# Kernel tuning notes

Hardware: AMD Instinct MI355X
Metric: run time of the kernel (lower is better)

Reference implementation:

```python
import jax, jax.numpy as jnp
import numpy as np

B, S, H, P = 8, 2048, 256, 64
NQ = 20

def setup_inputs() -> dict:
    key = jax.random.key(0)
    ks = jax.random.split(key, 12)
    s = lambda fan_in: 1.0 / np.sqrt(fan_in)
    return {
        "feature_x": jax.random.normal(ks[0], (B, S, H), dtype=jnp.float32),
        "param_x": jax.random.normal(ks[1], (B, S, P), dtype=jnp.float32),
        "sim_w1": jax.random.uniform(ks[2], (H, H // 2), jnp.float32, -s(H), s(H)),
        "sim_b1": jax.random.uniform(ks[3], (H // 2,), jnp.float32, -s(H), s(H)),
        "sim_w2": jax.random.uniform(ks[4], (H // 2, 1), jnp.float32, -s(H // 2), s(H // 2)),
        "sim_b2": jax.random.uniform(ks[5], (1,), jnp.float32, -s(H // 2), s(H // 2)),
        "conf_w1": jax.random.uniform(ks[6], (H, H // 2), jnp.float32, -s(H), s(H)),
        "conf_b1": jax.random.uniform(ks[7], (H // 2,), jnp.float32, -s(H), s(H)),
        "conf_w2": jax.random.uniform(ks[8], (H // 2, 1), jnp.float32, -s(H // 2), s(H // 2)),
        "conf_b2": jax.random.uniform(ks[9], (1,), jnp.float32, -s(H // 2), s(H // 2)),
        "questions": jax.random.randint(ks[10], (B, S), 0, NQ, dtype=jnp.int64 if jax.config.jax_enable_x64 else jnp.int32),
    }

def _mlp_scalar(x, w1, b1, w2, b2):
    # [B,S,H] -> [B,S] (dropout is eval-mode identity)
    h = jax.nn.relu(jnp.einsum("bsh,hk->bsk", x, w1) + b1)
    return (jnp.einsum("bsk,ko->bso", h, w2) + b2)[..., 0]

def reference(feature_x, param_x, sim_w1, sim_b1, sim_w2, sim_b2,
              conf_w1, conf_b1, conf_w2, conf_b2, questions):
    similarities = _mlp_scalar(feature_x, sim_w1, sim_b1, sim_w2, sim_b2)          # [B,S]
    confidences = jax.nn.sigmoid(_mlp_scalar(feature_x, conf_w1, conf_b1, conf_w2, conf_b2))  # [B,S]
    # multiplicative equality mask (zeros, not -inf, outside group — faithful to source)
    qmask = (questions[:, :, None] == questions[:, None, :]).astype(feature_x.dtype)  # [B,S,S]
    logits = similarities[:, :, None] * qmask                                        # [B,i,j]
    attn = jax.nn.softmax(logits, axis=-2)                                           # softmax over i
    smoothed = jnp.einsum("bij,bip->bjp", attn, param_x)                              # attn^T @ param_x
    c = confidences[..., None]
    return c * param_x + (1.0 - c) * smoothed
```

## Files before the change

### kernel.cpp

```cpp
#include <hip/hip_runtime.h>
#include <math.h>

#define B_  8
#define S_  2048
#define H_  256
#define HK_ 128
#define P_  64
#define NQ_ 20
#define M_  (B_*S_)
#define ACC_STRIDE 2688

#define WS_SIM   0
#define WS_CONF  16384
#define WS_ACC   32768
#define WS_WT    54272

typedef __attribute__((ext_vector_type(8))) short bf16x8;
typedef __attribute__((ext_vector_type(4))) float f32x4;

__global__ void prep_kernel(const float* __restrict__ sw1, const float* __restrict__ cw1,
                            short* __restrict__ wtf, float* __restrict__ ws_acc)
{
    const int t = blockIdx.x * 256 + threadIdx.x;
    const int l = t & 63, nt = (t >> 6) & 7, kt = (t >> 9) & 7, mlp = t >> 12;
    const int col = l & 15, quad = l >> 4;
    const int n = nt * 16 + col;
    const float* w1 = mlp ? cw1 : sw1;
    short frag[8];
    #pragma unroll
    for (int j = 0; j < 8; ++j) {
        int k = kt * 32 + quad * 8 + j;
        union { float f; unsigned u; } c; c.f = w1[k * HK_ + n];
        frag[j] = (short)((c.u + 0x7FFF + ((c.u >> 16) & 1)) >> 16);
    }
    *(uint4*)(wtf + (size_t)t * 8) = *(const uint4*)frag;
    for (int s = t; s < B_ * ACC_STRIDE; s += 8192) ws_acc[s] = 0.f;
}

__launch_bounds__(256)
__global__ void mlp_mfma_kernel(const float* __restrict__ fx, const short* __restrict__ wtf,
                                const float* __restrict__ sb1, const float* __restrict__ sw2,
                                const float* __restrict__ sb2, const float* __restrict__ cb1,
                                const float* __restrict__ cw2, const float* __restrict__ cb2,
                                float* __restrict__ sim, float* __restrict__ conf)
{
    const int tid  = threadIdx.x;
    const int w    = tid >> 6, l = tid & 63;
    const int col  = l & 15, quad = l >> 4;
    const int mlp  = w >> 1, mt = w & 1;
    const int row  = blockIdx.x * 32 + mt * 16 + col;

    f32x4 acc[8];
    #pragma unroll
    for (int nt = 0; nt < 8; ++nt) acc[nt] = (f32x4){0.f, 0.f, 0.f, 0.f};

    const float* fxrow = fx + (size_t)row * H_;
    const short* wf = wtf + (size_t)mlp * 32768 + (size_t)l * 8;

    #pragma unroll
    for (int kt = 0; kt < 8; ++kt) {
        float4 a0 = *(const float4*)(fxrow + kt * 32 + quad * 8);
        float4 a1 = *(const float4*)(fxrow + kt * 32 + quad * 8 + 4);
        float af[8] = {a0.x, a0.y, a0.z, a0.w, a1.x, a1.y, a1.z, a1.w};
        bf16x8 ahi, alo;
        #pragma unroll
        for (int i = 0; i < 8; ++i) {
            union { float f; unsigned u; } c; c.f = af[i];
            unsigned hi = c.u >> 16;
            ahi[i] = (short)hi;
            union { float f; unsigned u; } h2; h2.u = hi << 16;
            union { float f; unsigned u; } c2; c2.f = af[i] - h2.f;
            alo[i] = (short)(c2.u >> 16);
        }
        const short* base = wf + (size_t)kt * 4096;
        #pragma unroll
        for (int nt = 0; nt < 8; ++nt) {
            bf16x8 bf = *(const bf16x8*)(base + nt * 512);
            acc[nt] = __builtin_amdgcn_mfma_f32_16x16x32_bf16(ahi, bf, acc[nt], 0, 0, 0);
            acc[nt] = __builtin_amdgcn_mfma_f32_16x16x32_bf16(alo, bf, acc[nt], 0, 0, 0);
        }
    }

    const float* b1 = mlp ? cb1 : sb1;
    const float* w2 = mlp ? cw2 : sw2;
    const float  b2v = mlp ? cb2[0] : sb2[0];
    float p[4] = {0.f, 0.f, 0.f, 0.f};
    #pragma unroll
    for (int nt = 0; nt < 8; ++nt) {
        float b1c = b1[nt * 16 + col];
        float w2c = w2[nt * 16 + col];
        #pragma unroll
        for (int j = 0; j < 4; ++j)
            p[j] += fmaxf(acc[nt][j] + b1c, 0.f) * w2c;
    }
    #pragma unroll
    for (int off = 8; off >= 1; off >>= 1)
        #pragma unroll
        for (int j = 0; j < 4; ++j) p[j] += __shfl_down(p[j], off, 16);

    if (col == 0) {
        #pragma unroll
        for (int j = 0; j < 4; ++j) {
            int r = blockIdx.x * 32 + mt * 16 + quad * 4 + j;
            float v = p[j] + b2v;
            if (mlp == 0) sim[r] = v;
            else          conf[r] = 1.0f / (1.0f + expf(-v));
        }
    }
}

__launch_bounds__(256)
__global__ void accum_kernel(const float* __restrict__ sim, const int* __restrict__ questions,
                             const float* __restrict__ px, float* __restrict__ ws_acc)
{
    const int b = blockIdx.x;
    const int chunk = blockIdx.y;
    const int tid = threadIdx.x;
    const int lane = tid & 63;
    const int g = tid >> 6;
    __shared__ float accs[4][ACC_STRIDE];
    for (int s = tid; s < 4 * ACC_STRIDE; s += 256) ((float*)accs)[s] = 0.f;
    __syncthreads();

    const float* simb = sim + b * S_;
    const int*   qb   = questions + b * S_;
    const float* pxb  = px + (size_t)b * S_ * P_;

    float Treg = 0.f;
    const int i0 = chunk * 64 + g;
    for (int t = 0; t < 16; ++t) {
        int i = i0 + 4 * t;
        int qi = qb[i];
        float e = expf(simb[i]);
        float v = pxb[(size_t)i * P_ + lane];
        Treg += v;
        accs[g][qi * 64 + lane]        += v;
        accs[g][(20 + qi) * 64 + lane] += e * v;
        if (lane == 0) {
            accs[g][2624 + qi] += e;
            accs[g][2644 + qi] += 1.0f;
        }
    }
    accs[g][2560 + lane] += Treg;
    __syncthreads();

    float* dst = ws_acc + (size_t)b * ACC_STRIDE;
    for (int s = tid; s < ACC_STRIDE; s += 256) {
        float sum = accs[0][s] + accs[1][s] + accs[2][s] + accs[3][s];
        atomicAdd(dst + s, sum);
    }
}

__global__ void output_kernel(const float* __restrict__ px, const float* __restrict__ conf,
                              const int* __restrict__ questions, const float* __restrict__ ws_acc,
                              float* __restrict__ out)
{
    const int idx = blockIdx.x * 256 + threadIdx.x;
    const int row = idx >> 4;
    const int p4  = idx & 15;
    const int b   = row >> 11;
    const float c = conf[row];
    const int   q = questions[row];
    const float* accb = ws_acc + (size_t)b * ACC_STRIDE;
    const float4 T = *(const float4*)(accb + 2560 + p4 * 4);
    const float4 G = *(const float4*)(accb + q * 64 + p4 * 4);
    const float4 E = *(const float4*)(accb + (20 + q) * 64 + p4 * 4);
    const float denom = ((float)S_ - accb[2644 + q]) + accb[2624 + q];
    const float inv = 1.0f / denom;
    const float4 pv = ((const float4*)px)[idx];
    const float om = 1.0f - c;
    float4 o;
    o.x = c * pv.x + om * ((T.x - G.x + E.x) * inv);
    o.y = c * pv.y + om * ((T.y - G.y + E.y) * inv);
    o.z = c * pv.z + om * ((T.z - G.z + E.z) * inv);
    o.w = c * pv.w + om * ((T.w - G.w + E.w) * inv);
    ((float4*)out)[idx] = o;
}

extern "C" void kernel_launch(void* const* d_in, const int* in_sizes, int n_in,
                              void* d_out, int out_size, void* d_ws, size_t ws_size,
                              hipStream_t stream) {
    const float* fx  = (const float*)d_in[0];
    const float* px  = (const float*)d_in[1];
    const float* sw1 = (const float*)d_in[2];
    const float* sb1 = (const float*)d_in[3];
    const float* sw2 = (const float*)d_in[4];
    const float* sb2 = (const float*)d_in[5];
    const float* cw1 = (const float*)d_in[6];
    const float* cb1 = (const float*)d_in[7];
    const float* cw2 = (const float*)d_in[8];
    const float* cb2 = (const float*)d_in[9];
    const int* questions = (const int*)d_in[10];
    float* out = (float*)d_out;

    float* ws     = (float*)d_ws;
    float* sim    = ws + WS_SIM;
    float* conf   = ws + WS_CONF;
    float* ws_acc = ws + WS_ACC;
    short* wtf    = (short*)(ws + WS_WT);

    prep_kernel<<<32, 256, 0, stream>>>(sw1, cw1, wtf, ws_acc);
    mlp_mfma_kernel<<<M_ / 32, 256, 0, stream>>>(fx, wtf, sb1, sw2, sb2,
                                                 cb1, cw2, cb2, sim, conf);
    accum_kernel<<<dim3(B_, 32), 256, 0, stream>>>(sim, questions, px, ws_acc);
    output_kernel<<<(M_ * P_ / 4) / 256, 256, 0, stream>>>(px, conf, questions,
                                                           ws_acc, out);
}
```

Before: 109.9 us.

## Fuse MLP scoring with per-question accumulation into one kernel

Merges the MLP MFMA kernel and the accumulation kernel, so each block computes exp(similarity) for its 32 rows in shared memory and then accumulates param_x into a block-local per-question table. This drops the sim buffer round trip and one kernel launch. Global atomic flushes skip question slots that the block never touched. In exchange there are 512 blocks each doing global atomics (instead of 256), shared-memory atomics in place of per-wave private accumulators, and an extra barrier after the MLP.

```diff
diff --git a/kernel.cpp b/kernel.cpp
--- a/kernel.cpp
+++ b/kernel.cpp
@@ -10,10 +10,9 @@
 #define M_  (B_*S_)
 #define ACC_STRIDE 2688
 
-#define WS_SIM   0
-#define WS_CONF  16384
-#define WS_ACC   32768
-#define WS_WT    54272
+#define WS_CONF  0
+#define WS_ACC   16384
+#define WS_WT    37888
 
 typedef __attribute__((ext_vector_type(8))) short bf16x8;
 typedef __attribute__((ext_vector_type(4))) float f32x4;
@@ -38,17 +37,25 @@
 }
 
 __launch_bounds__(256)
-__global__ void mlp_mfma_kernel(const float* __restrict__ fx, const short* __restrict__ wtf,
-                                const float* __restrict__ sb1, const float* __restrict__ sw2,
-                                const float* __restrict__ sb2, const float* __restrict__ cb1,
-                                const float* __restrict__ cw2, const float* __restrict__ cb2,
-                                float* __restrict__ sim, float* __restrict__ conf)
+__global__ void mlp_accum_kernel(const float* __restrict__ fx, const short* __restrict__ wtf,
+                                 const float* __restrict__ px, const int* __restrict__ questions,
+                                 const float* __restrict__ sb1, const float* __restrict__ sw2,
+                                 const float* __restrict__ sb2, const float* __restrict__ cb1,
+                                 const float* __restrict__ cw2, const float* __restrict__ cb2,
+                                 float* __restrict__ conf_g, float* __restrict__ ws_acc)
 {
-    const int tid  = threadIdx.x;
-    const int w    = tid >> 6, l = tid & 63;
-    const int col  = l & 15, quad = l >> 4;
-    const int mlp  = w >> 1, mt = w & 1;
-    const int row  = blockIdx.x * 32 + mt * 16 + col;
+    const int tid = threadIdx.x;
+    const int bid = blockIdx.x;
+    const int w   = tid >> 6, l = tid & 63;
+    const int col = l & 15, quad = l >> 4;
+    const int mlp = w >> 1, mt = w & 1;
+    const int row = bid * 32 + mt * 16 + col;
+
+    __shared__ float accs[ACC_STRIDE];
+    __shared__ float ev[32];
+    __shared__ int   qflag[NQ_];
+    for (int s = tid; s < ACC_STRIDE; s += 256) accs[s] = 0.f;
+    if (tid < NQ_) qflag[tid] = 0;
 
     f32x4 acc[8];
     #pragma unroll
@@ -101,53 +108,44 @@
     if (col == 0) {
         #pragma unroll
         for (int j = 0; j < 4; ++j) {
-            int r = blockIdx.x * 32 + mt * 16 + quad * 4 + j;
+            int rl = mt * 16 + quad * 4 + j;
             float v = p[j] + b2v;
-            if (mlp == 0) sim[r] = v;
-            else          conf[r] = 1.0f / (1.0f + expf(-v));
-        }
-    }
-}
-
-__launch_bounds__(256)
-__global__ void accum_kernel(const float* __restrict__ sim, const int* __restrict__ questions,
-                             const float* __restrict__ px, float* __restrict__ ws_acc)
-{
-    const int b = blockIdx.x;
-    const int chunk = blockIdx.y;
-    const int tid = threadIdx.x;
-    const int lane = tid & 63;
-    const int g = tid >> 6;
-    __shared__ float accs[4][ACC_STRIDE];
-    for (int s = tid; s < 4 * ACC_STRIDE; s += 256) ((float*)accs)[s] = 0.f;
+            if (mlp == 0) ev[rl] = expf(v);
+            else          conf_g[bid * 32 + rl] = 1.0f / (1.0f + expf(-v));
+        }
+    }
     __syncthreads();
 
-    const float* simb = sim + b * S_;
-    const int*   qb   = questions + b * S_;
-    const float* pxb  = px + (size_t)b * S_ * P_;
+    const int b = bid >> 6;
+    const int i_s0 = (bid & 63) * 32;
+    const int* qb = questions + b * S_;
+    const float* pxb = px + (size_t)b * S_ * P_;
 
     float Treg = 0.f;
-    const int i0 = chunk * 64 + g;
-    for (int t = 0; t < 16; ++t) {
-        int i = i0 + 4 * t;
-        int qi = qb[i];
-        float e = expf(simb[i]);
-        float v = pxb[(size_t)i * P_ + lane];
+    #pragma unroll
+    for (int t = 0; t < 8; ++t) {
+        int rl = w * 8 + t;
+        int i_s = i_s0 + rl;
+        int qi = qb[i_s];
+        float e = ev[rl];
+        float v = pxb[(size_t)i_s * P_ + l];
         Treg += v;
-        accs[g][qi * 64 + lane]        += v;
-        accs[g][(20 + qi) * 64 + lane] += e * v;
-        if (lane == 0) {
-            accs[g][2624 + qi] += e;
-            accs[g][2644 + qi] += 1.0f;
-        }
-    }
-    accs[g][2560 + lane] += Treg;
+        atomicAdd(&accs[qi * 64 + l], v);
+        atomicAdd(&accs[1280 + qi * 64 + l], e * v);
+        if (l == 0) {
+            atomicAdd(&accs[2624 + qi], e);
+            atomicAdd(&accs[2644 + qi], 1.0f);
+            qflag[qi] = 1;
+        }
+    }
+    atomicAdd(&accs[2560 + l], Treg);
     __syncthreads();
 
     float* dst = ws_acc + (size_t)b * ACC_STRIDE;
     for (int s = tid; s < ACC_STRIDE; s += 256) {
-        float sum = accs[0][s] + accs[1][s] + accs[2][s] + accs[3][s];
-        atomicAdd(dst + s, sum);
+        int q = (s < 1280) ? (s >> 6) : (s < 2560) ? ((s - 1280) >> 6) : -1;
+        if (q >= 0 && !qflag[q]) continue;
+        atomicAdd(dst + s, accs[s]);
     }
 }
 
@@ -194,15 +192,14 @@
     float* out = (float*)d_out;
 
     float* ws     = (float*)d_ws;
-    float* sim    = ws + WS_SIM;
     float* conf   = ws + WS_CONF;
     float* ws_acc = ws + WS_ACC;
     short* wtf    = (short*)(ws + WS_WT);
 
     prep_kernel<<<32, 256, 0, stream>>>(sw1, cw1, wtf, ws_acc);
-    mlp_mfma_kernel<<<M_ / 32, 256, 0, stream>>>(fx, wtf, sb1, sw2, sb2,
-                                                 cb1, cw2, cb2, sim, conf);
-    accum_kernel<<<dim3(B_, 32), 256, 0, stream>>>(sim, questions, px, ws_acc);
+    mlp_accum_kernel<<<M_ / 32, 256, 0, stream>>>(fx, wtf, px, questions,
+                                                  sb1, sw2, sb2, cb1, cw2, cb2,
+                                                  conf, ws_acc);
     output_kernel<<<(M_ * P_ / 4) / 256, 256, 0, stream>>>(px, conf, questions,
                                                            ws_acc, out);
 }
```

New measurement: 113.8 us. +3.5%, slower.

## Process two row tiles per wave in MLP and coarsen accum blocks

Applied to the files above, without the earlier changes.

The MLP kernel now has each wave compute two 16-row tiles, so every bf16 weight fragment load is reused across 32 rows and the grid is halved. The accumulation kernel moves to a 1D grid of 64 blocks, each covering 256 rows instead of 64, which cuts the number of shared-memory initialisations and global atomic flushes by a factor of four. The cost is more registers per thread in the MLP kernel, which may lower occupancy, and less parallelism in the accumulation pass.

```diff
diff --git a/kernel.cpp b/kernel.cpp
--- a/kernel.cpp
+++ b/kernel.cpp
@@ -45,66 +45,86 @@
                                 float* __restrict__ sim, float* __restrict__ conf)
 {
     const int tid  = threadIdx.x;
+    const int bid  = blockIdx.x;
     const int w    = tid >> 6, l = tid & 63;
     const int col  = l & 15, quad = l >> 4;
-    const int mlp  = w >> 1, mt = w & 1;
-    const int row  = blockIdx.x * 32 + mt * 16 + col;
-
-    f32x4 acc[8];
-    #pragma unroll
-    for (int nt = 0; nt < 8; ++nt) acc[nt] = (f32x4){0.f, 0.f, 0.f, 0.f};
-
-    const float* fxrow = fx + (size_t)row * H_;
+    const int mlp  = w >> 1, half = w & 1;
+    const int r0   = bid * 64 + half * 32;
+
+    f32x4 acc0[8], acc1[8];
+    #pragma unroll
+    for (int nt = 0; nt < 8; ++nt) {
+        acc0[nt] = (f32x4){0.f, 0.f, 0.f, 0.f};
+        acc1[nt] = (f32x4){0.f, 0.f, 0.f, 0.f};
+    }
+
+    const float* fxrow0 = fx + (size_t)(r0 + col) * H_;
+    const float* fxrow1 = fx + (size_t)(r0 + 16 + col) * H_;
     const short* wf = wtf + (size_t)mlp * 32768 + (size_t)l * 8;
 
     #pragma unroll
     for (int kt = 0; kt < 8; ++kt) {
-        float4 a0 = *(const float4*)(fxrow + kt * 32 + quad * 8);
-        float4 a1 = *(const float4*)(fxrow + kt * 32 + quad * 8 + 4);
-        float af[8] = {a0.x, a0.y, a0.z, a0.w, a1.x, a1.y, a1.z, a1.w};
-        bf16x8 ahi, alo;
-        #pragma unroll
-        for (int i = 0; i < 8; ++i) {
-            union { float f; unsigned u; } c; c.f = af[i];
-            unsigned hi = c.u >> 16;
-            ahi[i] = (short)hi;
-            union { float f; unsigned u; } h2; h2.u = hi << 16;
-            union { float f; unsigned u; } c2; c2.f = af[i] - h2.f;
-            alo[i] = (short)(c2.u >> 16);
+        bf16x8 ahi[2], alo[2];
+        #pragma unroll
+        for (int rt = 0; rt < 2; ++rt) {
+            const float* fr = rt ? fxrow1 : fxrow0;
+            float4 a0 = *(const float4*)(fr + kt * 32 + quad * 8);
+            float4 a1 = *(const float4*)(fr + kt * 32 + quad * 8 + 4);
+            float af[8] = {a0.x, a0.y, a0.z, a0.w, a1.x, a1.y, a1.z, a1.w};
+            #pragma unroll
+            for (int i = 0; i < 8; ++i) {
+                union { float f; unsigned u; } c; c.f = af[i];
+                unsigned hi = c.u >> 16;
+                ahi[rt][i] = (short)hi;
+                union { float f; unsigned u; } h2; h2.u = hi << 16;
+                union { float f; unsigned u; } c2; c2.f = af[i] - h2.f;
+                alo[rt][i] = (short)(c2.u >> 16);
+            }
         }
         const short* base = wf + (size_t)kt * 4096;
         #pragma unroll
         for (int nt = 0; nt < 8; ++nt) {
             bf16x8 bf = *(const bf16x8*)(base + nt * 512);
-            acc[nt] = __builtin_amdgcn_mfma_f32_16x16x32_bf16(ahi, bf, acc[nt], 0, 0, 0);
-            acc[nt] = __builtin_amdgcn_mfma_f32_16x16x32_bf16(alo, bf, acc[nt], 0, 0, 0);
+            acc0[nt] = __builtin_amdgcn_mfma_f32_16x16x32_bf16(ahi[0], bf, acc0[nt], 0, 0, 0);
+            acc0[nt] = __builtin_amdgcn_mfma_f32_16x16x32_bf16(alo[0], bf, acc0[nt], 0, 0, 0);
+            acc1[nt] = __builtin_amdgcn_mfma_f32_16x16x32_bf16(ahi[1], bf, acc1[nt], 0, 0, 0);
+            acc1[nt] = __builtin_amdgcn_mfma_f32_16x16x32_bf16(alo[1], bf, acc1[nt], 0, 0, 0);
         }
     }
 
     const float* b1 = mlp ? cb1 : sb1;
     const float* w2 = mlp ? cw2 : sw2;
     const float  b2v = mlp ? cb2[0] : sb2[0];
-    float p[4] = {0.f, 0.f, 0.f, 0.f};
+    float p0[4] = {0.f, 0.f, 0.f, 0.f};
+    float p1[4] = {0.f, 0.f, 0.f, 0.f};
     #pragma unroll
     for (int nt = 0; nt < 8; ++nt) {
         float b1c = b1[nt * 16 + col];
         float w2c = w2[nt * 16 + col];
         #pragma unroll
-        for (int j = 0; j < 4; ++j)
-            p[j] += fmaxf(acc[nt][j] + b1c, 0.f) * w2c;
+        for (int j = 0; j < 4; ++j) {
+            p0[j] += fmaxf(acc0[nt][j] + b1c, 0.f) * w2c;
+            p1[j] += fmaxf(acc1[nt][j] + b1c, 0.f) * w2c;
+        }
     }
     #pragma unroll
     for (int off = 8; off >= 1; off >>= 1)
         #pragma unroll
-        for (int j = 0; j < 4; ++j) p[j] += __shfl_down(p[j], off, 16);
+        for (int j = 0; j < 4; ++j) {
+            p0[j] += __shfl_down(p0[j], off, 16);
+            p1[j] += __shfl_down(p1[j], off, 16);
+        }
 
     if (col == 0) {
         #pragma unroll
         for (int j = 0; j < 4; ++j) {
-            int r = blockIdx.x * 32 + mt * 16 + quad * 4 + j;
-            float v = p[j] + b2v;
-            if (mlp == 0) sim[r] = v;
-            else          conf[r] = 1.0f / (1.0f + expf(-v));
+            int ra = r0 + quad * 4 + j;
+            int rb = ra + 16;
+            float va = p0[j] + b2v;
+            float vb = p1[j] + b2v;
+            if (mlp == 0) { sim[ra] = va; sim[rb] = vb; }
+            else { conf[ra] = 1.0f / (1.0f + expf(-va));
+                   conf[rb] = 1.0f / (1.0f + expf(-vb)); }
         }
     }
 }
@@ -113,8 +133,8 @@
 __global__ void accum_kernel(const float* __restrict__ sim, const int* __restrict__ questions,
                              const float* __restrict__ px, float* __restrict__ ws_acc)
 {
-    const int b = blockIdx.x;
-    const int chunk = blockIdx.y;
+    const int b = blockIdx.x >> 3;
+    const int chunk = blockIdx.x & 7;
     const int tid = threadIdx.x;
     const int lane = tid & 63;
     const int g = tid >> 6;
@@ -127,8 +147,8 @@
     const float* pxb  = px + (size_t)b * S_ * P_;
 
     float Treg = 0.f;
-    const int i0 = chunk * 64 + g;
-    for (int t = 0; t < 16; ++t) {
+    const int i0 = chunk * 256 + g;
+    for (int t = 0; t < 64; ++t) {
         int i = i0 + 4 * t;
         int qi = qb[i];
         float e = expf(simb[i]);
@@ -200,9 +220,9 @@
     short* wtf    = (short*)(ws + WS_WT);
 
     prep_kernel<<<32, 256, 0, stream>>>(sw1, cw1, wtf, ws_acc);
-    mlp_mfma_kernel<<<M_ / 32, 256, 0, stream>>>(fx, wtf, sb1, sw2, sb2,
+    mlp_mfma_kernel<<<M_ / 64, 256, 0, stream>>>(fx, wtf, sb1, sw2, sb2,
                                                  cb1, cw2, cb2, sim, conf);
-    accum_kernel<<<dim3(B_, 32), 256, 0, stream>>>(sim, questions, px, ws_acc);
+    accum_kernel<<<B_ * 8, 256, 0, stream>>>(sim, questions, px, ws_acc);
     output_kernel<<<(M_ * P_ / 4) / 256, 256, 0, stream>>>(px, conf, questions,
                                                            ws_acc, out);
 }
```

Result: slower. 122.4 us (+11.3%).
